# Optimization experiments

Measured on AMD Instinct MI355X. Metric: run time of the kernel, lower is better.

## Reference

```python
import jax, jax.numpy as jnp
import numpy as np

N = 50000        # nodes
E = 1_600_000    # edges (avg degree 32)
F_IN = 128       # node feature dim
H = 64           # hidden_channels
C = 19           # output classes
G = 512          # graphs in the batch


def setup_inputs() -> dict:
    key = jax.random.key(0)
    ks = jax.random.split(key, 9)
    x = jax.random.normal(ks[0], (N, F_IN), dtype=jnp.float32)
    edge_index = jax.random.randint(ks[1], (2, E), 0, N, dtype=jnp.int64)
    batch = jnp.sort(jax.random.randint(ks[2], (N,), 0, G, dtype=jnp.int64))
    W1 = jax.random.normal(ks[3], (F_IN, H), dtype=jnp.float32) / np.sqrt(F_IN)
    b1 = jnp.zeros((H,), dtype=jnp.float32)
    W2 = jax.random.normal(ks[4], (H, H), dtype=jnp.float32) / np.sqrt(H)
    b2 = jnp.zeros((H,), dtype=jnp.float32)
    W_out = jax.random.normal(ks[5], (H, C), dtype=jnp.float32) / np.sqrt(H)
    b_out = jnp.zeros((C,), dtype=jnp.float32)
    return {"x": x, "edge_index": edge_index, "batch": batch,
            "W1": W1, "b1": b1, "W2": W2, "b2": b2,
            "W_out": W_out, "b_out": b_out}


def _gcn_conv(x, src, dst, W, b, n_nodes):
    """PyG GCNConv: add self-loops, symmetric D^-1/2 (A+I) D^-1/2 norm,
    linear transform first, gather-scale-scatter aggregation, then bias."""
    x = x @ W  # [N, out]
    loop = jnp.arange(n_nodes, dtype=src.dtype)
    s = jnp.concatenate([src, loop])  # source (message origin)
    d = jnp.concatenate([dst, loop])  # target (aggregation site)
    deg = jax.ops.segment_sum(jnp.ones_like(d, dtype=x.dtype), d,
                              num_segments=n_nodes)
    dinv = jnp.where(deg > 0, jax.lax.rsqrt(deg), 0.0)
    norm = dinv[s] * dinv[d]                       # [E+N]
    msg = x[s] * norm[:, None]                     # gather + scale
    out = jax.ops.segment_sum(msg, d, num_segments=n_nodes)  # scatter-add
    return out + b


def reference(x, edge_index, batch, W1, b1, W2, b2, W_out, b_out):
    src, dst = edge_index[0], edge_index[1]
    h = _gcn_conv(x, src, dst, W1, b1, N)
    h = jax.nn.relu(h)
    # F.dropout(training=False) -> identity (eval mode)
    h = _gcn_conv(h, src, dst, W2, b2, N)
    # global mean pool over graphs
    sums = jax.ops.segment_sum(h, batch, num_segments=G)        # [G, H]
    cnts = jax.ops.segment_sum(jnp.ones((N,), h.dtype), batch,
                               num_segments=G)                  # [G]
    pooled = sums / jnp.maximum(cnts, 1.0)[:, None]
    return pooled @ W_out + b_out                               # [G, C]
```

## Files before the change

kernel.cpp:

```cpp
#include <hip/hip_runtime.h>
#include <hip/hip_bf16.h>

#define F_IN 128
#define HID  64
#define NCLS 19
#define BW   128
#define NBMAX 512
#define ACAP 3072
#define BKCAP 5120
#define W1STR 136
#define W2STR 72

typedef __bf16 bf16x8 __attribute__((ext_vector_type(8)));
typedef float  f32x4  __attribute__((ext_vector_type(4)));

__device__ __forceinline__ float ldf(const void* p, long i, int fp32) {
    if (fp32) return ((const float*)p)[i];
    return __bfloat162float(((const __hip_bfloat16*)p)[i]);
}
__device__ __forceinline__ int ldi(const void* p, long i, int i64) {
    if (i64) return (int)((const long long*)p)[i];
    return ((const int*)p)[i];
}
__device__ __forceinline__ unsigned short f2bf(float f) {
    __hip_bfloat16 h = __float2bfloat16(f);
    unsigned short r;
    __builtin_memcpy(&r, &h, 2);
    return r;
}
__device__ __forceinline__ float bflo(unsigned u) { return __uint_as_float(u << 16); }
__device__ __forceinline__ float bfhi(unsigned u) { return __uint_as_float(u & 0xffff0000u); }

__device__ __forceinline__ bf16x8 ldfrag(const unsigned short* p) {
    uint4 u = *(const uint4*)p;
    return __builtin_bit_cast(bf16x8, u);
}
__device__ __forceinline__ bf16x8 ldfrag_any(const void* p, long off, int fp32) {
    if (!fp32) return ldfrag((const unsigned short*)p + off);
    const float4* f = (const float4*)((const float*)p + off);
    float4 u0 = f[0];
    float4 u1 = f[1];
    uint4 u = make_uint4((unsigned)f2bf(u0.x) | ((unsigned)f2bf(u0.y) << 16),
                         (unsigned)f2bf(u0.z) | ((unsigned)f2bf(u0.w) << 16),
                         (unsigned)f2bf(u1.x) | ((unsigned)f2bf(u1.y) << 16),
                         (unsigned)f2bf(u1.z) | ((unsigned)f2bf(u1.w) << 16));
    return __builtin_bit_cast(bf16x8, u);
}

__global__ __launch_bounds__(512) void k_detect(const void* x, const void* ei, int* flags,
                                                int* __restrict__ bcur, int NB) {
    int t = threadIdx.x;
    for (int b = t; b < NB; b += 512) bcur[b] = b * BKCAP;
    if (t != 0) return;
    const unsigned* xw = (const unsigned*)x;
    int bf16 = 1;
    for (int i = 0; i < 16; ++i) {
        unsigned w = xw[i];
        int elo = (w >> 7) & 0xFF;
        int ehi = (w >> 23) & 0xFF;
        if (elo < 100 || elo > 140 || ehi < 100 || ehi > 140) bf16 = 0;
    }
    const unsigned* iw = (const unsigned*)ei;
    int i64 = 1; unsigned anyev = 0;
    for (int k = 0; k < 8; ++k) {
        if (iw[2 * k + 1] != 0) i64 = 0;
        anyev |= iw[2 * k];
    }
    if (anyev == 0) i64 = 0;
    flags[0] = bf16 ? 0 : 1;
    flags[1] = i64;
}

__global__ __launch_bounds__(256) void k_bounds(const void* __restrict__ batch, int N, int G,
                                                int* __restrict__ bounds,
                                                const int* __restrict__ flags) {
    int i64 = flags[1];
    int i = blockIdx.x * 256 + threadIdx.x;
    if (i >= N) return;
    int b = min(max(ldi(batch, i, i64), 0), G - 1);
    int p = (i == 0) ? -1 : min(max(ldi(batch, (long)i - 1, i64), 0), G - 1);
    for (int g = p + 1; g <= b; ++g) bounds[g] = i;
    if (i == N - 1)
        for (int g = b + 1; g <= G; ++g) bounds[g] = N;
}

__global__ __launch_bounds__(512) void k_sortA(const void* __restrict__ ei, int E, int nbuck,
                                               int* bcur, int* __restrict__ bkt,
                                               const int* __restrict__ flags) {
    __shared__ int lbuf[ACAP];
    __shared__ unsigned short lbkt[ACAP];
    __shared__ int lh[NBMAX];
    __shared__ int lsc[NBMAX];
    __shared__ int lcur[NBMAX];
    __shared__ int gbase[NBMAX];
    __shared__ int wpart[8];
    int i64 = flags[1];
    int t = threadIdx.x;
    int e0 = blockIdx.x * ACAP;
    int e1 = min(E, e0 + ACAP);
    int cnt = e1 - e0;
    lh[t] = 0;
    __syncthreads();
    for (int e = e0 + t; e < e1; e += 512)
        atomicAdd(&lh[(ldi(ei, (long)E + e, i64) >> 7) & (NBMAX - 1)], 1);
    __syncthreads();
    int v = lh[t];
    int lane = t & 63, wq = t >> 6;
    int incl = v;
#pragma unroll
    for (int off = 1; off < 64; off <<= 1) {
        int n = __shfl_up(incl, off);
        if (lane >= off) incl += n;
    }
    if (lane == 63) wpart[wq] = incl;
    __syncthreads();
    if (t == 0) {
        int acc = 0;
#pragma unroll
        for (int i = 0; i < 8; ++i) { int xx = wpart[i]; wpart[i] = acc; acc += xx; }
    }
    __syncthreads();
    int ex = wpart[wq] + incl - v;
    lsc[t] = ex;
    lcur[t] = ex;
    gbase[t] = (v && t < nbuck) ? atomicAdd(&bcur[t], v) : 0;
    __syncthreads();
    for (int e = e0 + t; e < e1; e += 512) {
        int s = ldi(ei, e, i64);
        int d = ldi(ei, (long)E + e, i64);
        int b = (d >> 7) & (NBMAX - 1);
        int r = atomicAdd(&lcur[b], 1);
        r = min(max(r, 0), ACAP - 1);
        lbuf[r] = (s << 7) | (d & (BW - 1));
        lbkt[r] = (unsigned short)b;
    }
    __syncthreads();
    for (int i = t; i < cnt; i += 512) {
        int lo = lbkt[i];
        int idx = gbase[lo] + (i - lsc[lo]);
        if (idx >= lo * BKCAP && idx < (lo + 1) * BKCAP) bkt[idx] = lbuf[i];
    }
}

__global__ __launch_bounds__(512) void k_sortB(const int* __restrict__ bkt,
                                               const int* __restrict__ bcur,
                                               int N,
                                               int* __restrict__ csr,
                                               int* __restrict__ cursor,
                                               int* __restrict__ deg,
                                               float* __restrict__ dinv) {
    __shared__ int lstage[BKCAP];
    __shared__ int lcsr[BKCAP];
    __shared__ int lh[BW], lsc[BW], lcur[BW];
    int b = blockIdx.x, t = threadIdx.x;
    int base = b * BKCAP;
    int cnt = min(max(bcur[b] - base, 0), BKCAP);
    if (t < BW) lh[t] = 0;
    __syncthreads();
    for (int i = t; i < cnt; i += 512) {
        int w = __builtin_nontemporal_load(&bkt[base + i]);
        lstage[i] = w;
        atomicAdd(&lh[w & (BW - 1)], 1);
    }
    __syncthreads();
    if (t < BW) lsc[t] = lh[t];
    __syncthreads();
    for (int off = 1; off < BW; off <<= 1) {
        int a = (t < BW && t >= off) ? lsc[t - off] : 0;
        __syncthreads();
        if (t < BW) lsc[t] += a;
        __syncthreads();
    }
    if (t < BW) {
        int ex = lsc[t] - lh[t];
        lcur[t] = ex;
        int n = b * BW + t;
        if (n < N) {
            cursor[n] = base + ex;
            deg[n] = lh[t];
            dinv[n] = rsqrtf((float)(lh[t] + 1));
        }
    }
    __syncthreads();
    for (int i = t; i < cnt; i += 512) {
        int w = lstage[i];
        int r = atomicAdd(&lcur[w & (BW - 1)], 1);
        int sv = (int)((unsigned)w >> 7);
        if (sv >= N) sv = 0;
        r = min(max(r, 0), BKCAP - 1);
        lcsr[r] = sv;
    }
    __syncthreads();
    for (int i = t; i < cnt; i += 512) csr[base + i] = lcsr[i];
}

__global__ __launch_bounds__(256) void k_gemm1(const void* __restrict__ x,
                                               const void* __restrict__ W,
                                               const float* __restrict__ dinv,
                                               unsigned short* __restrict__ t, int N,
                                               const int* __restrict__ flags) {
    __shared__ __align__(16) unsigned short wt[HID * W1STR];
    int fp32 = flags[0];
    int tid = threadIdx.x;
    if (fp32) {
        const float* wf = (const float*)W;
        for (int i = tid * 4; i < F_IN * HID; i += 1024) {
            float4 w4 = *(const float4*)(wf + i);
            int k = i >> 6, n = i & 63;
            wt[(n + 0) * W1STR + k] = f2bf(w4.x);
            wt[(n + 1) * W1STR + k] = f2bf(w4.y);
            wt[(n + 2) * W1STR + k] = f2bf(w4.z);
            wt[(n + 3) * W1STR + k] = f2bf(w4.w);
        }
    } else {
        for (int i = tid; i < F_IN * HID; i += 256) {
            int k = i >> 6, n = i & 63;
            wt[n * W1STR + k] = f2bf(ldf(W, i, 0));
        }
    }
    __syncthreads();
    int wv = tid >> 6, lane = tid & 63;
    int quad = lane >> 4, l16 = lane & 15;
    int r0 = blockIdx.x * 64 + wv * 16;
    int rowA = min(r0 + l16, N - 1);
    bf16x8 a[4];
#pragma unroll
    for (int kq = 0; kq < 4; ++kq)
        a[kq] = ldfrag_any(x, (long)rowA * F_IN + kq * 32 + quad * 8, fp32);
    float di[4];
    int rowC = r0 + quad * 4;
#pragma unroll
    for (int r = 0; r < 4; ++r) di[r] = (rowC + r < N) ? dinv[rowC + r] : 0.f;
#pragma unroll
    for (int cg = 0; cg < 4; ++cg) {
        int col = cg * 16 + l16;
        f32x4 acc = {0.f, 0.f, 0.f, 0.f};
#pragma unroll
        for (int kq = 0; kq < 4; ++kq) {
            bf16x8 b = ldfrag(wt + col * W1STR + kq * 32 + quad * 8);
            acc = __builtin_amdgcn_mfma_f32_16x16x32_bf16(a[kq], b, acc, 0, 0, 0);
        }
#pragma unroll
        for (int r = 0; r < 4; ++r) {
            int row = rowC + r;
            if (row < N) t[(size_t)row * HID + col] = f2bf(di[r] * acc[r]);
        }
    }
}

__global__ __launch_bounds__(256) void k_gemm2(const unsigned short* __restrict__ h,
                                               const void* __restrict__ W,
                                               const float* __restrict__ dinv,
                                               unsigned short* __restrict__ t, int N,
                                               const int* __restrict__ flags) {
    __shared__ __align__(16) unsigned short wt[HID * W2STR];
    int fp32 = flags[0];
    int tid = threadIdx.x;
    if (fp32) {
        const float* wf = (const float*)W;
        for (int i = tid * 4; i < HID * HID; i += 1024) {
            float4 w4 = *(const float4*)(wf + i);
            int k = i >> 6, n = i & 63;
            wt[(n + 0) * W2STR + k] = f2bf(w4.x);
            wt[(n + 1) * W2STR + k] = f2bf(w4.y);
            wt[(n + 2) * W2STR + k] = f2bf(w4.z);
            wt[(n + 3) * W2STR + k] = f2bf(w4.w);
        }
    } else {
        for (int i = tid; i < HID * HID; i += 256) {
            int k = i >> 6, n = i & 63;
            wt[n * W2STR + k] = f2bf(ldf(W, i, 0));
        }
    }
    __syncthreads();
    int wv = tid >> 6, lane = tid & 63;
    int quad = lane >> 4, l16 = lane & 15;
    int r0 = blockIdx.x * 64 + wv * 16;
    int rowA = min(r0 + l16, N - 1);
    bf16x8 a[2];
#pragma unroll
    for (int kq = 0; kq < 2; ++kq)
        a[kq] = ldfrag(h + (size_t)rowA * HID + kq * 32 + quad * 8);
    float di[4];
    int rowC = r0 + quad * 4;
#pragma unroll
    for (int r = 0; r < 4; ++r) di[r] = (rowC + r < N) ? dinv[rowC + r] : 0.f;
#pragma unroll
    for (int cg = 0; cg < 4; ++cg) {
        int col = cg * 16 + l16;
        f32x4 acc = {0.f, 0.f, 0.f, 0.f};
#pragma unroll
        for (int kq = 0; kq < 2; ++kq) {
            bf16x8 b = ldfrag(wt + col * W2STR + kq * 32 + quad * 8);
            acc = __builtin_amdgcn_mfma_f32_16x16x32_bf16(a[kq], b, acc, 0, 0, 0);
        }
#pragma unroll
        for (int r = 0; r < 4; ++r) {
            int row = rowC + r;
            if (row < N) t[(size_t)row * HID + col] = f2bf(di[r] * acc[r]);
        }
    }
}

template <bool RELU>
__global__ __launch_bounds__(256) void k_agg(const unsigned short* __restrict__ t,
                                             const int* __restrict__ csr,
                                             const int* __restrict__ cursor,
                                             const int* __restrict__ deg,
                                             const float* __restrict__ dinv,
                                             const void* __restrict__ bias,
                                             unsigned short* __restrict__ out,
                                             int N, int SZ, const int* __restrict__ flags) {
    __shared__ float sbias[HID];
    __shared__ int scur[8];
    __shared__ int sdeg[8];
    __shared__ float sdv[8];
    int tid = threadIdx.x;
    int nb = blockIdx.x * 8;
    if (tid < HID) sbias[tid] = ldf(bias, tid, flags[0]);
    if (tid >= 64 && tid < 72) {
        int q = tid - 64;
        int node = nb + q;
        int c = 0, d = 0;
        float dv = 0.f;
        if (node < N) { c = cursor[node]; d = deg[node]; dv = dinv[node]; }
        scur[q] = c; sdeg[q] = d; sdv[q] = dv;
    }
    __syncthreads();
    int wv = tid >> 6, lane = tid & 63;
    int half = lane >> 5;
    int idx = wv * 2 + half;
    int node = nb + idx;
    int l = lane & 31;
    int g = l >> 3;
    int l8 = (l & 7) * 8;
    bool alive = (node < N);
    int snode = alive ? node : 0;
    int beg = scur[idx];
    int dg = sdeg[idx];
    beg = min(max(beg, 0), SZ);
    int end = beg + min(max(dg, 0), SZ - beg);
    uint4 sv = make_uint4(0u, 0u, 0u, 0u);
    if (g == 0) sv = *(const uint4*)(t + (size_t)snode * HID + l8);
    float a0 = 0.f, a1 = 0.f, a2 = 0.f, a3 = 0.f;
    float a4 = 0.f, a5 = 0.f, a6 = 0.f, a7 = 0.f;
    int e = beg;
    for (; e + 32 <= end; e += 32) {
        int s[8];
#pragma unroll
        for (int k = 0; k < 8; ++k) {
            int si = __builtin_nontemporal_load(&csr[e + 4 * k + g]);
            s[k] = ((unsigned)si < (unsigned)N) ? si : 0;
        }
        uint4 v[8];
#pragma unroll
        for (int k = 0; k < 8; ++k)
            v[k] = *(const uint4*)(t + (size_t)s[k] * HID + l8);
#pragma unroll
        for (int k = 0; k < 8; ++k) {
            a0 += bflo(v[k].x); a1 += bfhi(v[k].x);
            a2 += bflo(v[k].y); a3 += bfhi(v[k].y);
            a4 += bflo(v[k].z); a5 += bfhi(v[k].z);
            a6 += bflo(v[k].w); a7 += bfhi(v[k].w);
        }
    }
    if (e < end) {
        int s[8];
#pragma unroll
        for (int k = 0; k < 8; ++k) {
            int i = e + 4 * k + g;
            int si = __builtin_nontemporal_load(&csr[i < end ? i : end - 1]);
            s[k] = ((unsigned)si < (unsigned)N) ? si : 0;
        }
        uint4 v[8];
#pragma unroll
        for (int k = 0; k < 8; ++k)
            v[k] = *(const uint4*)(t + (size_t)s[k] * HID + l8);
#pragma unroll
        for (int k = 0; k < 8; ++k) {
            if (e + 4 * k + g < end) {
                a0 += bflo(v[k].x); a1 += bfhi(v[k].x);
                a2 += bflo(v[k].y); a3 += bfhi(v[k].y);
                a4 += bflo(v[k].z); a5 += bfhi(v[k].z);
                a6 += bflo(v[k].w); a7 += bfhi(v[k].w);
            }
        }
    }
#pragma unroll
    for (int m = 8; m <= 16; m <<= 1) {
        a0 += __shfl_xor(a0, m); a1 += __shfl_xor(a1, m);
        a2 += __shfl_xor(a2, m); a3 += __shfl_xor(a3, m);
        a4 += __shfl_xor(a4, m); a5 += __shfl_xor(a5, m);
        a6 += __shfl_xor(a6, m); a7 += __shfl_xor(a7, m);
    }
    if (g == 0 && alive) {
        a0 += bflo(sv.x); a1 += bfhi(sv.x); a2 += bflo(sv.y); a3 += bfhi(sv.y);
        a4 += bflo(sv.z); a5 += bfhi(sv.z); a6 += bflo(sv.w); a7 += bfhi(sv.w);
        float di = sdv[idx];
        float v0 = di * a0 + sbias[l8 + 0];
        float v1 = di * a1 + sbias[l8 + 1];
        float v2 = di * a2 + sbias[l8 + 2];
        float v3 = di * a3 + sbias[l8 + 3];
        float v4 = di * a4 + sbias[l8 + 4];
        float v5 = di * a5 + sbias[l8 + 5];
        float v6 = di * a6 + sbias[l8 + 6];
        float v7 = di * a7 + sbias[l8 + 7];
        if (RELU) {
            v0 = fmaxf(v0, 0.f); v1 = fmaxf(v1, 0.f); v2 = fmaxf(v2, 0.f); v3 = fmaxf(v3, 0.f);
            v4 = fmaxf(v4, 0.f); v5 = fmaxf(v5, 0.f); v6 = fmaxf(v6, 0.f); v7 = fmaxf(v7, 0.f);
        }
        uint4 pk;
        pk.x = (unsigned)f2bf(v0) | ((unsigned)f2bf(v1) << 16);
        pk.y = (unsigned)f2bf(v2) | ((unsigned)f2bf(v3) << 16);
        pk.z = (unsigned)f2bf(v4) | ((unsigned)f2bf(v5) << 16);
        pk.w = (unsigned)f2bf(v6) | ((unsigned)f2bf(v7) << 16);
        *(uint4*)(out + (size_t)node * HID + l8) = pk;
    }
}

__global__ __launch_bounds__(256) void k_poolout(const unsigned short* __restrict__ h2,
                                                 const int* __restrict__ bounds, int N,
                                                 const void* __restrict__ Wout,
                                                 const void* __restrict__ bout,
                                                 void* __restrict__ out,
                                                 const int* __restrict__ flags) {
    __shared__ float pr[HID];
    __shared__ float sacc[4][HID];
    int g = blockIdx.x;
    int start = min(max(bounds[g], 0), N);
    int endg = min(max(bounds[g + 1], start), N);
    int tid = threadIdx.x;
    int wv = tid >> 6, lane = tid & 63;
    int half = lane >> 5;
    int l = lane & 31;
    float s0 = 0.f, s1 = 0.f;
    for (int r = start + wv * 2 + half; r < endg; r += 8) {
        unsigned u = *(const unsigned*)(h2 + (size_t)r * HID + 2 * l);
        s0 += bflo(u);
        s1 += bfhi(u);
    }
    s0 += __shfl_xor(s0, 32);
    s1 += __shfl_xor(s1, 32);
    if (lane < 32) {
        sacc[wv][2 * l] = s0;
        sacc[wv][2 * l + 1] = s1;
    }
    __syncthreads();
    if (tid < HID) {
        float inv = 1.f / fmaxf((float)(endg - start), 1.f);
        pr[tid] = (sacc[0][tid] + sacc[1][tid] + sacc[2][tid] + sacc[3][tid]) * inv;
    }
    __syncthreads();
    int fp32 = flags[0];
    if (tid < NCLS) {
        float acc = ldf(bout, tid, fp32);
#pragma unroll 4
        for (int k = 0; k < HID; ++k)
            acc += pr[k] * ldf(Wout, k * NCLS + tid, fp32);
        if (fp32) ((float*)out)[g * NCLS + tid] = acc;
        else ((__hip_bfloat16*)out)[g * NCLS + tid] = __float2bfloat16(acc);
    }
}

extern "C" void kernel_launch(void* const* d_in, const int* in_sizes, int n_in,
                              void* d_out, int out_size, void* d_ws, size_t ws_size,
                              hipStream_t stream) {
    const void* x    = d_in[0];
    const void* ei   = d_in[1];
    const void* bat  = d_in[2];
    const void* W1   = d_in[3];
    const void* b1   = d_in[4];
    const void* W2   = d_in[5];
    const void* b2   = d_in[6];
    const void* Wout = d_in[7];
    const void* bout = d_in[8];

    const int N = in_sizes[0] / F_IN;
    const int E = in_sizes[1] / 2;
    const int G = out_size / NCLS;
    const int NB = (N + BW - 1) / BW;
    const int SZ = NB * BKCAP;

    char* ws = (char*)d_ws;
    size_t off = 0;
    auto carve = [&](size_t bytes) -> void* {
        void* p = ws + off;
        off = (off + bytes + 255) & ~(size_t)255;
        return p;
    };
    int*            flags  = (int*)carve(64);
    int*            deg    = (int*)carve((size_t)N * 4);
    int*            cursor = (int*)carve((size_t)N * 4);
    float*          dinv   = (float*)carve((size_t)N * 4);
    int*            bcur   = (int*)carve((size_t)NB * 4);
    int*            bounds = (int*)carve((size_t)(G + 1) * 4);
    int*            csr    = (int*)carve((size_t)SZ * 4);
    int*            bkt    = (int*)carve((size_t)SZ * 4);
    unsigned short* t      = (unsigned short*)carve((size_t)N * HID * 2);
    unsigned short* h      = (unsigned short*)carve((size_t)N * HID * 2);
    (void)ws_size; (void)n_in;

    k_detect<<<1, 512, 0, stream>>>(x, ei, flags, bcur, NB);
    k_bounds<<<(N + 255) / 256, 256, 0, stream>>>(bat, N, G, bounds, flags);

    int na = (E + ACAP - 1) / ACAP;
    k_sortA<<<na, 512, 0, stream>>>(ei, E, NB, bcur, bkt, flags);
    k_sortB<<<NB, 512, 0, stream>>>(bkt, bcur, N, csr, cursor, deg, dinv);

    int gb = (N + 63) / 64;
    int ab = (N + 7) / 8;
    k_gemm1<<<gb, 256, 0, stream>>>(x, W1, dinv, t, N, flags);
    k_agg<true><<<ab, 256, 0, stream>>>(t, csr, cursor, deg, dinv, b1, h, N, SZ, flags);
    k_gemm2<<<gb, 256, 0, stream>>>(h, W2, dinv, t, N, flags);
    k_agg<false><<<ab, 256, 0, stream>>>(t, csr, cursor, deg, dinv, b2, h, N, SZ, flags);
    k_poolout<<<G, 256, 0, stream>>>(h, bounds, N, Wout, bout, d_out, flags);
}
```

Baseline: 204.9 us.

## Split feature table into column halves and aggregate each half separately

Stores the intermediate node features as two contiguous N×32 column halves instead of N×64 rows, and runs the gather-aggregate kernel once per half. The aim is to shrink the randomly-gathered working set so it fits in L2 cache, reducing DRAM traffic from scattered neighbour reads. In exchange, edge indices are read twice, gathers use 8-byte instead of 16-byte accesses, and extra kernel launches are added. The GEMM kernels are also changed to process 128 rows per block and write the split layout.

```diff
diff --git a/kernel.cpp b/kernel.cpp
--- a/kernel.cpp
+++ b/kernel.cpp
@@ -202,6 +202,7 @@
     __shared__ __align__(16) unsigned short wt[HID * W1STR];
     int fp32 = flags[0];
     int tid = threadIdx.x;
+    size_t N32 = (size_t)N * 32;
     if (fp32) {
         const float* wf = (const float*)W;
         for (int i = tid * 4; i < F_IN * HID; i += 1024) {
@@ -221,29 +222,34 @@
     __syncthreads();
     int wv = tid >> 6, lane = tid & 63;
     int quad = lane >> 4, l16 = lane & 15;
-    int r0 = blockIdx.x * 64 + wv * 16;
-    int rowA = min(r0 + l16, N - 1);
-    bf16x8 a[4];
-#pragma unroll
-    for (int kq = 0; kq < 4; ++kq)
-        a[kq] = ldfrag_any(x, (long)rowA * F_IN + kq * 32 + quad * 8, fp32);
-    float di[4];
-    int rowC = r0 + quad * 4;
-#pragma unroll
-    for (int r = 0; r < 4; ++r) di[r] = (rowC + r < N) ? dinv[rowC + r] : 0.f;
-#pragma unroll
-    for (int cg = 0; cg < 4; ++cg) {
-        int col = cg * 16 + l16;
-        f32x4 acc = {0.f, 0.f, 0.f, 0.f};
-#pragma unroll
-        for (int kq = 0; kq < 4; ++kq) {
-            bf16x8 b = ldfrag(wt + col * W1STR + kq * 32 + quad * 8);
-            acc = __builtin_amdgcn_mfma_f32_16x16x32_bf16(a[kq], b, acc, 0, 0, 0);
-        }
-#pragma unroll
-        for (int r = 0; r < 4; ++r) {
-            int row = rowC + r;
-            if (row < N) t[(size_t)row * HID + col] = f2bf(di[r] * acc[r]);
+#pragma unroll
+    for (int rr = 0; rr < 128; rr += 64) {
+        int r0 = blockIdx.x * 128 + rr + wv * 16;
+        if (r0 >= N) break;
+        int rowA = min(r0 + l16, N - 1);
+        bf16x8 a[4];
+#pragma unroll
+        for (int kq = 0; kq < 4; ++kq)
+            a[kq] = ldfrag_any(x, (long)rowA * F_IN + kq * 32 + quad * 8, fp32);
+        float di[4];
+        int rowC = r0 + quad * 4;
+#pragma unroll
+        for (int r = 0; r < 4; ++r) di[r] = (rowC + r < N) ? dinv[rowC + r] : 0.f;
+#pragma unroll
+        for (int cg = 0; cg < 4; ++cg) {
+            int col = cg * 16 + l16;
+            f32x4 acc = {0.f, 0.f, 0.f, 0.f};
+#pragma unroll
+            for (int kq = 0; kq < 4; ++kq) {
+                bf16x8 b = ldfrag(wt + col * W1STR + kq * 32 + quad * 8);
+                acc = __builtin_amdgcn_mfma_f32_16x16x32_bf16(a[kq], b, acc, 0, 0, 0);
+            }
+            unsigned short* tp = t + (size_t)(col >> 5) * N32 + (col & 31);
+#pragma unroll
+            for (int r = 0; r < 4; ++r) {
+                int row = rowC + r;
+                if (row < N) tp[(size_t)row * 32] = f2bf(di[r] * acc[r]);
+            }
         }
     }
 }
@@ -256,6 +262,7 @@
     __shared__ __align__(16) unsigned short wt[HID * W2STR];
     int fp32 = flags[0];
     int tid = threadIdx.x;
+    size_t N32 = (size_t)N * 32;
     if (fp32) {
         const float* wf = (const float*)W;
         for (int i = tid * 4; i < HID * HID; i += 1024) {
@@ -275,34 +282,39 @@
     __syncthreads();
     int wv = tid >> 6, lane = tid & 63;
     int quad = lane >> 4, l16 = lane & 15;
-    int r0 = blockIdx.x * 64 + wv * 16;
-    int rowA = min(r0 + l16, N - 1);
-    bf16x8 a[2];
-#pragma unroll
-    for (int kq = 0; kq < 2; ++kq)
-        a[kq] = ldfrag(h + (size_t)rowA * HID + kq * 32 + quad * 8);
-    float di[4];
-    int rowC = r0 + quad * 4;
-#pragma unroll
-    for (int r = 0; r < 4; ++r) di[r] = (rowC + r < N) ? dinv[rowC + r] : 0.f;
-#pragma unroll
-    for (int cg = 0; cg < 4; ++cg) {
-        int col = cg * 16 + l16;
-        f32x4 acc = {0.f, 0.f, 0.f, 0.f};
-#pragma unroll
-        for (int kq = 0; kq < 2; ++kq) {
-            bf16x8 b = ldfrag(wt + col * W2STR + kq * 32 + quad * 8);
-            acc = __builtin_amdgcn_mfma_f32_16x16x32_bf16(a[kq], b, acc, 0, 0, 0);
-        }
-#pragma unroll
-        for (int r = 0; r < 4; ++r) {
-            int row = rowC + r;
-            if (row < N) t[(size_t)row * HID + col] = f2bf(di[r] * acc[r]);
-        }
-    }
-}
-
-template <bool RELU>
+#pragma unroll
+    for (int rr = 0; rr < 128; rr += 64) {
+        int r0 = blockIdx.x * 128 + rr + wv * 16;
+        if (r0 >= N) break;
+        int rowA = min(r0 + l16, N - 1);
+        bf16x8 a[2];
+#pragma unroll
+        for (int kq = 0; kq < 2; ++kq)
+            a[kq] = ldfrag(h + (size_t)kq * N32 + (size_t)rowA * 32 + quad * 8);
+        float di[4];
+        int rowC = r0 + quad * 4;
+#pragma unroll
+        for (int r = 0; r < 4; ++r) di[r] = (rowC + r < N) ? dinv[rowC + r] : 0.f;
+#pragma unroll
+        for (int cg = 0; cg < 4; ++cg) {
+            int col = cg * 16 + l16;
+            f32x4 acc = {0.f, 0.f, 0.f, 0.f};
+#pragma unroll
+            for (int kq = 0; kq < 2; ++kq) {
+                bf16x8 b = ldfrag(wt + col * W2STR + kq * 32 + quad * 8);
+                acc = __builtin_amdgcn_mfma_f32_16x16x32_bf16(a[kq], b, acc, 0, 0, 0);
+            }
+            unsigned short* tp = t + (size_t)(col >> 5) * N32 + (col & 31);
+#pragma unroll
+            for (int r = 0; r < 4; ++r) {
+                int row = rowC + r;
+                if (row < N) tp[(size_t)row * 32] = f2bf(di[r] * acc[r]);
+            }
+        }
+    }
+}
+
+template <bool RELU, int FH>
 __global__ __launch_bounds__(256) void k_agg(const unsigned short* __restrict__ t,
                                              const int* __restrict__ csr,
                                              const int* __restrict__ cursor,
@@ -311,13 +323,13 @@
                                              const void* __restrict__ bias,
                                              unsigned short* __restrict__ out,
                                              int N, int SZ, const int* __restrict__ flags) {
-    __shared__ float sbias[HID];
+    __shared__ float sbias[32];
     __shared__ int scur[8];
     __shared__ int sdeg[8];
     __shared__ float sdv[8];
     int tid = threadIdx.x;
     int nb = blockIdx.x * 8;
-    if (tid < HID) sbias[tid] = ldf(bias, tid, flags[0]);
+    if (tid < 32) sbias[tid] = ldf(bias, FH * 32 + tid, flags[0]);
     if (tid >= 64 && tid < 72) {
         int q = tid - 64;
         int node = nb + q;
@@ -327,23 +339,25 @@
         scur[q] = c; sdeg[q] = d; sdv[q] = dv;
     }
     __syncthreads();
+    size_t N32 = (size_t)N * 32;
+    const unsigned short* tb = t + (size_t)FH * N32;
+    unsigned short* ob = out + (size_t)FH * N32;
     int wv = tid >> 6, lane = tid & 63;
     int half = lane >> 5;
     int idx = wv * 2 + half;
     int node = nb + idx;
     int l = lane & 31;
     int g = l >> 3;
-    int l8 = (l & 7) * 8;
+    int l4 = (l & 7) * 4;
     bool alive = (node < N);
     int snode = alive ? node : 0;
     int beg = scur[idx];
     int dg = sdeg[idx];
     beg = min(max(beg, 0), SZ);
     int end = beg + min(max(dg, 0), SZ - beg);
-    uint4 sv = make_uint4(0u, 0u, 0u, 0u);
-    if (g == 0) sv = *(const uint4*)(t + (size_t)snode * HID + l8);
+    uint2 sv = make_uint2(0u, 0u);
+    if (g == 0) sv = *(const uint2*)(tb + (size_t)snode * 32 + l4);
     float a0 = 0.f, a1 = 0.f, a2 = 0.f, a3 = 0.f;
-    float a4 = 0.f, a5 = 0.f, a6 = 0.f, a7 = 0.f;
     int e = beg;
     for (; e + 32 <= end; e += 32) {
         int s[8];
@@ -352,16 +366,14 @@
             int si = __builtin_nontemporal_load(&csr[e + 4 * k + g]);
             s[k] = ((unsigned)si < (unsigned)N) ? si : 0;
         }
-        uint4 v[8];
+        uint2 v[8];
 #pragma unroll
         for (int k = 0; k < 8; ++k)
-            v[k] = *(const uint4*)(t + (size_t)s[k] * HID + l8);
+            v[k] = *(const uint2*)(tb + (size_t)s[k] * 32 + l4);
 #pragma unroll
         for (int k = 0; k < 8; ++k) {
             a0 += bflo(v[k].x); a1 += bfhi(v[k].x);
             a2 += bflo(v[k].y); a3 += bfhi(v[k].y);
-            a4 += bflo(v[k].z); a5 += bfhi(v[k].z);
-            a6 += bflo(v[k].w); a7 += bfhi(v[k].w);
         }
     }
     if (e < end) {
@@ -372,17 +384,15 @@
             int si = __builtin_nontemporal_load(&csr[i < end ? i : end - 1]);
             s[k] = ((unsigned)si < (unsigned)N) ? si : 0;
         }
-        uint4 v[8];
+        uint2 v[8];
 #pragma unroll
         for (int k = 0; k < 8; ++k)
-            v[k] = *(const uint4*)(t + (size_t)s[k] * HID + l8);
+            v[k] = *(const uint2*)(tb + (size_t)s[k] * 32 + l4);
 #pragma unroll
         for (int k = 0; k < 8; ++k) {
             if (e + 4 * k + g < end) {
                 a0 += bflo(v[k].x); a1 += bfhi(v[k].x);
                 a2 += bflo(v[k].y); a3 += bfhi(v[k].y);
-                a4 += bflo(v[k].z); a5 += bfhi(v[k].z);
-                a6 += bflo(v[k].w); a7 += bfhi(v[k].w);
             }
         }
     }
@@ -390,31 +400,22 @@
     for (int m = 8; m <= 16; m <<= 1) {
         a0 += __shfl_xor(a0, m); a1 += __shfl_xor(a1, m);
         a2 += __shfl_xor(a2, m); a3 += __shfl_xor(a3, m);
-        a4 += __shfl_xor(a4, m); a5 += __shfl_xor(a5, m);
-        a6 += __shfl_xor(a6, m); a7 += __shfl_xor(a7, m);
     }
     if (g == 0 && alive) {
         a0 += bflo(sv.x); a1 += bfhi(sv.x); a2 += bflo(sv.y); a3 += bfhi(sv.y);
-        a4 += bflo(sv.z); a5 += bfhi(sv.z); a6 += bflo(sv.w); a7 += bfhi(sv.w);
         float di = sdv[idx];
-        float v0 = di * a0 + sbias[l8 + 0];
-        float v1 = di * a1 + sbias[l8 + 1];
-        float v2 = di * a2 + sbias[l8 + 2];
-        float v3 = di * a3 + sbias[l8 + 3];
-        float v4 = di * a4 + sbias[l8 + 4];
-        float v5 = di * a5 + sbias[l8 + 5];
-        float v6 = di * a6 + sbias[l8 + 6];
-        float v7 = di * a7 + sbias[l8 + 7];
+        float v0 = di * a0 + sbias[l4 + 0];
+        float v1 = di * a1 + sbias[l4 + 1];
+        float v2 = di * a2 + sbias[l4 + 2];
+        float v3 = di * a3 + sbias[l4 + 3];
         if (RELU) {
-            v0 = fmaxf(v0, 0.f); v1 = fmaxf(v1, 0.f); v2 = fmaxf(v2, 0.f); v3 = fmaxf(v3, 0.f);
-            v4 = fmaxf(v4, 0.f); v5 = fmaxf(v5, 0.f); v6 = fmaxf(v6, 0.f); v7 = fmaxf(v7, 0.f);
-        }
-        uint4 pk;
+            v0 = fmaxf(v0, 0.f); v1 = fmaxf(v1, 0.f);
+            v2 = fmaxf(v2, 0.f); v3 = fmaxf(v3, 0.f);
+        }
+        uint2 pk;
         pk.x = (unsigned)f2bf(v0) | ((unsigned)f2bf(v1) << 16);
         pk.y = (unsigned)f2bf(v2) | ((unsigned)f2bf(v3) << 16);
-        pk.z = (unsigned)f2bf(v4) | ((unsigned)f2bf(v5) << 16);
-        pk.w = (unsigned)f2bf(v6) | ((unsigned)f2bf(v7) << 16);
-        *(uint4*)(out + (size_t)node * HID + l8) = pk;
+        *(uint2*)(ob + (size_t)node * 32 + l4) = pk;
     }
 }
 
@@ -433,9 +434,11 @@
     int wv = tid >> 6, lane = tid & 63;
     int half = lane >> 5;
     int l = lane & 31;
+    size_t N32 = (size_t)N * 32;
+    const unsigned short* hb = h2 + (size_t)(l >> 4) * N32 + 2 * (l & 15);
     float s0 = 0.f, s1 = 0.f;
     for (int r = start + wv * 2 + half; r < endg; r += 8) {
-        unsigned u = *(const unsigned*)(h2 + (size_t)r * HID + 2 * l);
+        unsigned u = *(const unsigned*)(hb + (size_t)r * 32);
         s0 += bflo(u);
         s1 += bfhi(u);
     }
@@ -507,11 +510,13 @@
     k_sortA<<<na, 512, 0, stream>>>(ei, E, NB, bcur, bkt, flags);
     k_sortB<<<NB, 512, 0, stream>>>(bkt, bcur, N, csr, cursor, deg, dinv);
 
-    int gb = (N + 63) / 64;
+    int gb = (N + 127) / 128;
     int ab = (N + 7) / 8;
     k_gemm1<<<gb, 256, 0, stream>>>(x, W1, dinv, t, N, flags);
-    k_agg<true><<<ab, 256, 0, stream>>>(t, csr, cursor, deg, dinv, b1, h, N, SZ, flags);
+    k_agg<true, 0><<<ab, 256, 0, stream>>>(t, csr, cursor, deg, dinv, b1, h, N, SZ, flags);
+    k_agg<true, 1><<<ab, 256, 0, stream>>>(t, csr, cursor, deg, dinv, b1, h, N, SZ, flags);
     k_gemm2<<<gb, 256, 0, stream>>>(h, W2, dinv, t, N, flags);
-    k_agg<false><<<ab, 256, 0, stream>>>(t, csr, cursor, deg, dinv, b2, h, N, SZ, flags);
+    k_agg<false, 0><<<ab, 256, 0, stream>>>(t, csr, cursor, deg, dinv, b2, h, N, SZ, flags);
+    k_agg<false, 1><<<ab, 256, 0, stream>>>(t, csr, cursor, deg, dinv, b2, h, N, SZ, flags);
     k_poolout<<<G, 256, 0, stream>>>(h, bounds, N, Wout, bout, d_out, flags);
 }
```

New measurement: 237.0 us. 15.6% more time.
